# Kernel optimization log

Measured on AMD Instinct MI355X. Metric: run time of the kernel, lower is better.

## Reference

```python
import jax, jax.numpy as jnp
import numpy as np

D = 1024
NHEAD = 16
HEAD_DIM = D // NHEAD


def setup_inputs() -> dict:
    key = jax.random.key(0)
    ks = jax.random.split(key, 7)
    B, L = 4, 2048
    q = jax.random.normal(ks[0], (B, L, D), dtype=jnp.float32)
    k = jax.random.normal(ks[1], (B, L, D), dtype=jnp.float32)
    v = jax.random.normal(ks[2], (B, L, D), dtype=jnp.float32)
    # packed QKV projection, as in nn.MultiheadAttention (in_proj_weight: [3d, d])
    scale = 1.0 / np.sqrt(D)
    in_proj_w = jax.random.uniform(ks[3], (3 * D, D), dtype=jnp.float32, minval=-scale, maxval=scale)
    in_proj_b = jnp.zeros((3 * D,), dtype=jnp.float32)
    out_w = jax.random.uniform(ks[4], (D, D), dtype=jnp.float32, minval=-scale, maxval=scale)
    out_b = jnp.zeros((D,), dtype=jnp.float32)
    return {"q": q, "k": k, "v": v, "in_proj_w": in_proj_w, "in_proj_b": in_proj_b,
            "out_w": out_w, "out_b": out_b}


def reference(q, k, v, in_proj_w, in_proj_b, out_w, out_b):
    # FP32 MHA, need_weights=True (average over heads), eval mode (dropout inactive).
    B, Lq, d = q.shape
    Lk = k.shape[1]
    # packed in-projection: rows [0:d] -> Q, [d:2d] -> K, [2d:3d] -> V
    qp = q @ in_proj_w[:d].T + in_proj_b[:d]
    kp = k @ in_proj_w[d:2 * d].T + in_proj_b[d:2 * d]
    vp = v @ in_proj_w[2 * d:].T + in_proj_b[2 * d:]
    # split heads: [B, H, L, hd]
    qp = qp.reshape(B, Lq, NHEAD, HEAD_DIM).transpose(0, 2, 1, 3)
    kp = kp.reshape(B, Lk, NHEAD, HEAD_DIM).transpose(0, 2, 1, 3)
    vp = vp.reshape(B, Lk, NHEAD, HEAD_DIM).transpose(0, 2, 1, 3)
    scores = jnp.einsum('bhqd,bhkd->bhqk', qp, kp) / jnp.sqrt(jnp.float32(HEAD_DIM))
    attn = jax.nn.softmax(scores, axis=-1)          # [B, H, Lq, Lk]
    ctx = jnp.einsum('bhqk,bhkd->bhqd', attn, vp)    # [B, H, Lq, hd]
    ctx = ctx.transpose(0, 2, 1, 3).reshape(B, Lq, d)
    out = ctx @ out_w.T + out_b                      # [B, Lq, d]
    weights = attn.mean(axis=1)                      # average over heads -> [B, Lq, Lk]
    return out, weights
```

## Files before the change

### kernel.cpp

```cpp
#include <hip/hip_runtime.h>
#include <hip/hip_bf16.h>

#define D_ 1024
#define NH 16
#define HD 64
#define B_ 4
#define L_ 2048
#define N_ (B_*L_)
#define BH_ (B_*NH)
#define QSCALE_ 0.18033688011112042f

typedef __bf16 bf16_t;
typedef __bf16 bf16x4 __attribute__((ext_vector_type(4)));
typedef __bf16 bf16x8 __attribute__((ext_vector_type(8)));
typedef float f32x4 __attribute__((ext_vector_type(4)));

typedef const __attribute__((address_space(1))) char gas_t;
typedef __attribute__((address_space(3))) char las_t;

__device__ __forceinline__ f32x4 mfma_bf16(bf16x8 a, bf16x8 b, f32x4 c) {
    return __builtin_amdgcn_mfma_f32_16x16x32_bf16(a, b, c, 0, 0, 0);
}

__device__ __forceinline__ bf16x8 cvt8_f32(const float* __restrict__ p) {
    const float4* p4 = reinterpret_cast<const float4*>(p);
    float4 a = p4[0], b = p4[1];
    bf16x8 r;
    r[0] = (bf16_t)a.x; r[1] = (bf16_t)a.y; r[2] = (bf16_t)a.z; r[3] = (bf16_t)a.w;
    r[4] = (bf16_t)b.x; r[5] = (bf16_t)b.y; r[6] = (bf16_t)b.z; r[7] = (bf16_t)b.w;
    return r;
}

__device__ __forceinline__ bf16x8 ld8_bf16(const bf16_t* __restrict__ p) {
    return *reinterpret_cast<const bf16x8*>(p);
}

__global__ __launch_bounds__(256) void k_cvt_all(
    const float* __restrict__ s0, const float* __restrict__ s1,
    const float* __restrict__ s2, const float* __restrict__ sw,
    const float* __restrict__ so,
    bf16_t* __restrict__ d0, bf16_t* __restrict__ d1, bf16_t* __restrict__ d2,
    bf16_t* __restrict__ dw, bf16_t* __restrict__ dow)
{
    const int n8  = N_ * D_ / 8;
    const int n8w = 3 * D_ * D_ / 8;
    const int n8o = D_ * D_ / 8;
    const int tot = 3 * n8 + n8w + n8o;
    int i = blockIdx.x * blockDim.x + threadIdx.x;
    int stride = gridDim.x * blockDim.x;
    for (; i < tot; i += stride) {
        const float* s; bf16_t* d; int off;
        if (i < 3 * n8) {
            int seg = i >> 20; off = i & (n8 - 1);
            s = (seg == 0) ? s0 : ((seg == 1) ? s1 : s2);
            d = (seg == 0) ? d0 : ((seg == 1) ? d1 : d2);
        } else if (i < 3 * n8 + n8w) {
            off = i - 3 * n8; s = sw; d = dw;
        } else {
            off = i - 3 * n8 - n8w; s = so; d = dow;
        }
        *reinterpret_cast<bf16x8*>(d + (size_t)off * 8) = cvt8_f32(s + (size_t)off * 8);
    }
}

__global__ __launch_bounds__(256, 4) void k_gemm_qkv(
    const bf16_t* __restrict__ qb, const bf16_t* __restrict__ kb,
    const bf16_t* __restrict__ vb, const bf16_t* __restrict__ wb,
    const float* __restrict__ bias,
    bf16_t* __restrict__ qp, bf16_t* __restrict__ kp, bf16_t* __restrict__ vpT)
{
    __shared__ __align__(16) char ldsA[2][8192];
    __shared__ __align__(16) char ldsB[2][8192];
    int tid  = threadIdx.x;
    int lane = tid & 63, w = tid >> 6;
    int r = lane & 15, g = lane >> 4;
    int wr = w >> 1, wc = w & 1;

    int bid   = blockIdx.x;
    int xcd   = bid & 7;
    int seq   = bid >> 3;
    int sec   = seq >> 6;
    int inner = seq & 63;
    int tm  = xcd * 8 + (inner >> 3);
    int ctl = (inner & 7) * 128;

    const bf16_t* A = (sec == 0) ? qb : ((sec == 1) ? kb : vb);
    const bf16_t* Ab = A + (size_t)tm * 128 * 1024;
    const bf16_t* Bb = wb + (size_t)sec * D_ * D_ + (size_t)ctl * 1024;

    f32x4 z = {0.f, 0.f, 0.f, 0.f};
    f32x4 acc[4][4];
    #pragma unroll
    for (int m = 0; m < 4; ++m)
        #pragma unroll
        for (int n = 0; n < 4; ++n) acc[m][n] = z;

    auto stage = [&](int buf, int k0) {
        #pragma unroll
        for (int i = 0; i < 2; ++i) {
            int idx = i * 256 + tid;
            int row = idx >> 2;
            int lc  = (idx & 3) ^ ((row >> 1) & 3);
            const bf16_t* gA = Ab + (size_t)row * 1024 + k0 + lc * 8;
            const bf16_t* gB = Bb + (size_t)row * 1024 + k0 + lc * 8;
            __builtin_amdgcn_global_load_lds((gas_t*)gA,
                (las_t*)(&ldsA[buf][0] + idx * 16), 16, 0, 0);
            __builtin_amdgcn_global_load_lds((gas_t*)gB,
                (las_t*)(&ldsB[buf][0] + idx * 16), 16, 0, 0);
        }
    };

    stage(0, 0);
    stage(1, 32);
    int buf = 0;

    for (int k0 = 0; k0 < 1024; k0 += 32) {
        if (k0 < 992) asm volatile("s_waitcnt vmcnt(4)" ::: "memory");
        else          asm volatile("s_waitcnt vmcnt(0)" ::: "memory");
        __builtin_amdgcn_s_barrier();
        __builtin_amdgcn_sched_barrier(0);

        bf16x8 af[4], bf_[4];
        #pragma unroll
        for (int m = 0; m < 4; ++m) {
            int R = wr * 64 + m * 16 + r;
            af[m] = *reinterpret_cast<const bf16x8*>(
                &ldsA[buf][0] + R * 64 + (((g ^ ((R >> 1) & 3)) << 4)));
        }
        #pragma unroll
        for (int n = 0; n < 4; ++n) {
            int R = wc * 64 + n * 16 + r;
            bf_[n] = *reinterpret_cast<const bf16x8*>(
                &ldsB[buf][0] + R * 64 + (((g ^ ((R >> 1) & 3)) << 4)));
        }
        #pragma unroll
        for (int m = 0; m < 4; ++m)
            #pragma unroll
            for (int n = 0; n < 4; ++n)
                acc[m][n] = mfma_bf16(af[m], bf_[n], acc[m][n]);

        __builtin_amdgcn_s_barrier();
        if (k0 + 64 < 1024) stage(buf, k0 + 64);
        buf ^= 1;
    }

    #pragma unroll
    for (int m = 0; m < 4; ++m)
        #pragma unroll
        for (int n = 0; n < 4; ++n)
            #pragma unroll
            for (int i = 0; i < 4; ++i) {
                int row = tm * 128 + wr * 64 + m * 16 + g * 4 + i;
                int col = ctl + wc * 64 + n * 16 + r;
                float val = acc[m][n][i] + bias[sec * 1024 + col];
                int bb = row >> 11, ln = row & 2047;
                int h = col >> 6, dd = col & 63;
                if (sec == 0)
                    qp[(((size_t)(bb * NH + h)) * L_ + ln) * HD + dd] =
                        (bf16_t)(val * QSCALE_);
                else if (sec == 1)
                    kp[(((size_t)(bb * NH + h)) * L_ + ln) * HD + dd] = (bf16_t)val;
                else
                    vpT[(((size_t)(bb * NH + h)) * HD + dd) * L_ + ln] = (bf16_t)val;
            }
}

__global__ __launch_bounds__(256, 4) void k_gemm_out(
    const bf16_t* __restrict__ A, const bf16_t* __restrict__ Bm,
    const float* __restrict__ bias, float* __restrict__ dst)
{
    __shared__ __align__(16) char ldsA[2][8192];
    __shared__ __align__(16) char ldsB[2][8192];
    int tid  = threadIdx.x;
    int lane = tid & 63, w = tid >> 6;
    int r = lane & 15, g = lane >> 4;
    int wr = w >> 1, wc = w & 1;

    int bid = blockIdx.x;
    int swz = (bid & 7) * 64 + (bid >> 3);
    int tm = swz >> 3, tn = swz & 7;

    const bf16_t* Ab = A  + (size_t)tm * 128 * 1024;
    const bf16_t* Bb = Bm + (size_t)tn * 128 * 1024;

    f32x4 z = {0.f, 0.f, 0.f, 0.f};
    f32x4 acc[4][4];
    #pragma unroll
    for (int m = 0; m < 4; ++m)
        #pragma unroll
        for (int n = 0; n < 4; ++n) acc[m][n] = z;

    auto stage = [&](int buf, int k0) {
        #pragma unroll
        for (int i = 0; i < 2; ++i) {
            int idx = i * 256 + tid;
            int row = idx >> 2;
            int lc  = (idx & 3) ^ ((row >> 1) & 3);
            const bf16_t* gA = Ab + (size_t)row * 1024 + k0 + lc * 8;
            const bf16_t* gB = Bb + (size_t)row * 1024 + k0 + lc * 8;
            __builtin_amdgcn_global_load_lds((gas_t*)gA,
                (las_t*)(&ldsA[buf][0] + idx * 16), 16, 0, 0);
            __builtin_amdgcn_global_load_lds((gas_t*)gB,
                (las_t*)(&ldsB[buf][0] + idx * 16), 16, 0, 0);
        }
    };

    stage(0, 0);
    stage(1, 32);
    int buf = 0;

    for (int k0 = 0; k0 < 1024; k0 += 32) {
        if (k0 < 992) asm volatile("s_waitcnt vmcnt(4)" ::: "memory");
        else          asm volatile("s_waitcnt vmcnt(0)" ::: "memory");
        __builtin_amdgcn_s_barrier();
        __builtin_amdgcn_sched_barrier(0);

        bf16x8 af[4], bf_[4];
        #pragma unroll
        for (int m = 0; m < 4; ++m) {
            int R = wr * 64 + m * 16 + r;
            af[m] = *reinterpret_cast<const bf16x8*>(
                &ldsA[buf][0] + R * 64 + (((g ^ ((R >> 1) & 3)) << 4)));
        }
        #pragma unroll
        for (int n = 0; n < 4; ++n) {
            int R = wc * 64 + n * 16 + r;
            bf_[n] = *reinterpret_cast<const bf16x8*>(
                &ldsB[buf][0] + R * 64 + (((g ^ ((R >> 1) & 3)) << 4)));
        }
        #pragma unroll
        for (int m = 0; m < 4; ++m)
            #pragma unroll
            for (int n = 0; n < 4; ++n)
                acc[m][n] = mfma_bf16(af[m], bf_[n], acc[m][n]);

        __builtin_amdgcn_s_barrier();
        if (k0 + 64 < 1024) stage(buf, k0 + 64);
        buf ^= 1;
    }

    #pragma unroll
    for (int m = 0; m < 4; ++m)
        #pragma unroll
        for (int n = 0; n < 4; ++n)
            #pragma unroll
            for (int i = 0; i < 4; ++i) {
                int row = tm * 128 + wr * 64 + m * 16 + g * 4 + i;
                int col = tn * 128 + wc * 64 + n * 16 + r;
                dst[(size_t)row * 1024 + col] = acc[m][n][i] + bias[col];
            }
}

__global__ __launch_bounds__(256, 4) void k_attn(
    const bf16_t* __restrict__ qp, const bf16_t* __restrict__ kp,
    const bf16_t* __restrict__ vpT,
    bf16_t* __restrict__ ctx, float* __restrict__ lInvOut)
{
    __shared__ __align__(16) char sK[8192];
    __shared__ __align__(16) char sV[8192];
    __shared__ __align__(16) char sP[4][4096];

    int tid  = threadIdx.x;
    int w    = tid >> 6;
    int lane = tid & 63;
    int r = lane & 15, g = lane >> 4;
    int bh = blockIdx.x & 63;
    int qg = blockIdx.x >> 6;
    int qbase = qg * 128 + w * 32;

    const bf16_t* qpb = qp  + (size_t)bh * L_ * HD;
    const bf16_t* kpb = kp  + (size_t)bh * L_ * HD;
    const bf16_t* vtb = vpT + (size_t)bh * HD * L_;

    bf16x8 bq[2][2];
    #pragma unroll
    for (int qt = 0; qt < 2; ++qt)
        #pragma unroll
        for (int ds = 0; ds < 2; ++ds)
            bq[qt][ds] = ld8_bf16(qpb + (size_t)(qbase + qt * 16 + r) * HD + ds * 32 + g * 8);

    bf16x8 ones;
    #pragma unroll
    for (int i = 0; i < 8; ++i) ones[i] = (bf16_t)1.0f;

    f32x4 z = {0.f, 0.f, 0.f, 0.f};
    f32x4 acc[2][4];
    #pragma unroll
    for (int qt = 0; qt < 2; ++qt)
        #pragma unroll
        for (int dt = 0; dt < 4; ++dt) acc[qt][dt] = z;
    f32x4 acc_l[2];
    acc_l[0] = z; acc_l[1] = z;

    char* Pw = &sP[w][0];

    int srow = tid >> 3;
    int slc  = (tid & 7) ^ (srow & 7);
    const bf16_t* gK0 = kpb + (size_t)srow * HD + slc * 8;
    const bf16_t* gV0 = vtb + (size_t)srow * L_ + slc * 8;

    for (int kt = 0; kt < 32; ++kt) {
        int k0 = kt * 64;
        const bf16_t* gK = gK0 + (size_t)k0 * HD;
        const bf16_t* gV = gV0 + k0;
        #pragma unroll
        for (int i = 0; i < 2; ++i) {
            __builtin_amdgcn_global_load_lds((gas_t*)(gK + (size_t)i * 32 * HD),
                (las_t*)(&sK[0] + i * 4096 + tid * 16), 16, 0, 0);
            __builtin_amdgcn_global_load_lds((gas_t*)(gV + (size_t)i * 32 * L_),
                (las_t*)(&sV[0] + i * 4096 + tid * 16), 16, 0, 0);
        }
        __syncthreads();

        f32x4 sT[4][2];
        __builtin_amdgcn_s_setprio(1);
        #pragma unroll
        for (int ktile = 0; ktile < 4; ++ktile) {
            bf16x8 a0 = *reinterpret_cast<const bf16x8*>(
                &sK[0] + (ktile * 16 + r) * 128 + (((g    ) ^ (r & 7)) << 4));
            bf16x8 a1 = *reinterpret_cast<const bf16x8*>(
                &sK[0] + (ktile * 16 + r) * 128 + (((4 + g) ^ (r & 7)) << 4));
            #pragma unroll
            for (int qt = 0; qt < 2; ++qt) {
                f32x4 t = mfma_bf16(a0, bq[qt][0], z);
                sT[ktile][qt] = mfma_bf16(a1, bq[qt][1], t);
            }
        }
        __builtin_amdgcn_s_setprio(0);

        #pragma unroll
        for (int qt = 0; qt < 2; ++qt) {
            #pragma unroll
            for (int ktile = 0; ktile < 4; ++ktile) {
                bf16x4 pw;
                #pragma unroll
                for (int i = 0; i < 4; ++i)
                    pw[i] = (bf16_t)__builtin_amdgcn_exp2f(sT[ktile][qt][i]);
                *reinterpret_cast<bf16x4*>(Pw + (qt * 16 + r) * 128 +
                    (((2 * ktile + (g >> 1)) ^ (r & 7)) << 4) + ((g & 1) << 3)) = pw;
            }
        }

        bf16x8 pa[2][2];
        #pragma unroll
        for (int qt = 0; qt < 2; ++qt)
            #pragma unroll
            for (int ks = 0; ks < 2; ++ks)
                pa[qt][ks] = *reinterpret_cast<const bf16x8*>(
                    Pw + (qt * 16 + r) * 128 + (((4 * ks + g) ^ (r & 7)) << 4));
        __builtin_amdgcn_s_setprio(1);
        #pragma unroll
        for (int qt = 0; qt < 2; ++qt) {
            acc_l[qt] = mfma_bf16(pa[qt][0], ones, acc_l[qt]);
            acc_l[qt] = mfma_bf16(pa[qt][1], ones, acc_l[qt]);
        }
        #pragma unroll
        for (int dt = 0; dt < 4; ++dt)
            #pragma unroll
            for (int ks = 0; ks < 2; ++ks) {
                bf16x8 bv = *reinterpret_cast<const bf16x8*>(
                    &sV[0] + (dt * 16 + r) * 128 + (((4 * ks + g) ^ (r & 7)) << 4));
                acc[0][dt] = mfma_bf16(pa[0][ks], bv, acc[0][dt]);
                acc[1][dt] = mfma_bf16(pa[1][ks], bv, acc[1][dt]);
            }
        __builtin_amdgcn_s_setprio(0);

        __syncthreads();
    }

    int bb = bh >> 4, h = bh & 15;
    #pragma unroll
    for (int qt = 0; qt < 2; ++qt) {
        float lq[4];
        #pragma unroll
        for (int i = 0; i < 4; ++i) lq[i] = 1.0f / acc_l[qt][i];
        #pragma unroll
        for (int i = 0; i < 4; ++i) {
            int q = qbase + qt * 16 + 4 * g + i;
            #pragma unroll
            for (int dt = 0; dt < 4; ++dt) {
                float val = acc[qt][dt][i] * lq[i];
                ctx[(((size_t)(bb * L_ + q)) * NH + h) * HD + dt * 16 + r] = (bf16_t)val;
            }
        }
        if (r == 0) {
            #pragma unroll
            for (int i = 0; i < 4; ++i) {
                int q = qbase + qt * 16 + 4 * g + i;
                lInvOut[(size_t)bh * L_ + q] = lq[i];
            }
        }
    }
}

__global__ __launch_bounds__(256, 2) void k_weights(
    const bf16_t* __restrict__ qp, const bf16_t* __restrict__ kp,
    const float* __restrict__ lInv, float* __restrict__ wout)
{
    __shared__ __align__(16) char sQ[2][16384];
    __shared__ __align__(16) char sKt[2][16384];
    __shared__ __align__(16) float sLi[16][128];

    int tid  = threadIdx.x;
    int w    = tid >> 6;
    int lane = tid & 63;
    int r = lane & 15, g = lane >> 4;
    int wr = w >> 1, wc = w & 1;

    int wgid = (blockIdx.x & 7) * 128 + (blockIdx.x >> 3);
    int chunk = wgid >> 7;
    int b  = chunk >> 1;
    int qh = chunk & 1;
    int rem = wgid & 127;
    int qt = qh * 8 + (rem >> 4);
    int kt = rem & 15;
    int q0 = qt * 128, k0 = kt * 128;

    #pragma unroll
    for (int i = 0; i < 2; ++i) {
        int idx = i * 256 + tid;
        int h   = idx >> 5;
        int off = (idx & 31) * 4;
        const float* gl = lInv + ((size_t)(b * NH + h) * L_ + q0 + off);
        __builtin_amdgcn_global_load_lds((gas_t*)gl,
            (las_t*)((char*)&sLi[0][0] + i * 4096 + w * 1024), 16, 0, 0);
    }

    auto stage_qk = [&](int buf, int h) {
        const bf16_t* Qh = qp + ((size_t)(b * NH + h) * L_ + q0) * HD;
        const bf16_t* Kh = kp + ((size_t)(b * NH + h) * L_ + k0) * HD;
        #pragma unroll
        for (int i = 0; i < 4; ++i) {
            int idx = i * 256 + tid;
            int row = idx >> 3;
            int lc  = (idx & 7) ^ (row & 7);
            const bf16_t* gQ = Qh + (size_t)row * HD + lc * 8;
            const bf16_t* gK = Kh + (size_t)row * HD + lc * 8;
            __builtin_amdgcn_global_load_lds((gas_t*)gQ,
                (las_t*)(&sQ[buf][0]  + i * 4096 + w * 1024), 16, 0, 0);
            __builtin_amdgcn_global_load_lds((gas_t*)gK,
                (las_t*)(&sKt[buf][0] + i * 4096 + w * 1024), 16, 0, 0);
        }
    };

    float acc[4][4][4] = {};
    f32x4 z = {0.f, 0.f, 0.f, 0.f};

    stage_qk(0, 0);
    __syncthreads();
    int buf = 0;

    for (int h = 0; h < NH; ++h) {
        if (h + 1 < NH) stage_qk(buf ^ 1, h + 1);

        const char* Qb = &sQ[buf][0];
        const char* Kb = &sKt[buf][0];

        bf16x8 bfrag[4][2];
        #pragma unroll
        for (int nf = 0; nf < 4; ++nf) {
            int R = wc * 64 + nf * 16 + r;
            bfrag[nf][0] = *reinterpret_cast<const bf16x8*>(
                Kb + R * 128 + (((g    ) ^ (R & 7)) << 4));
            bfrag[nf][1] = *reinterpret_cast<const bf16x8*>(
                Kb + R * 128 + (((4 + g) ^ (R & 7)) << 4));
        }
        #pragma unroll
        for (int mf = 0; mf < 4; ++mf) {
            int R = wr * 64 + mf * 16 + r;
            bf16x8 af0 = *reinterpret_cast<const bf16x8*>(
                Qb + R * 128 + (((g    ) ^ (R & 7)) << 4));
            bf16x8 af1 = *reinterpret_cast<const bf16x8*>(
                Qb + R * 128 + (((4 + g) ^ (R & 7)) << 4));
            int qrow = wr * 64 + mf * 16 + g * 4;
            f32x4 liv = *reinterpret_cast<const f32x4*>(&sLi[h][qrow]);
            #pragma unroll
            for (int nf = 0; nf < 4; ++nf) {
                f32x4 t = mfma_bf16(af0, bfrag[nf][0], z);
                t = mfma_bf16(af1, bfrag[nf][1], t);
                #pragma unroll
                for (int i = 0; i < 4; ++i)
                    acc[mf][nf][i] += __builtin_amdgcn_exp2f(t[i]) * liv[i];
            }
        }
        __syncthreads();
        buf ^= 1;
    }

    const float inv_h = 1.0f / (float)NH;
    #pragma unroll
    for (int mf = 0; mf < 4; ++mf)
        #pragma unroll
        for (int nf = 0; nf < 4; ++nf)
            #pragma unroll
            for (int i = 0; i < 4; ++i) {
                int qidx = q0 + wr * 64 + mf * 16 + g * 4 + i;
                int kidx = k0 + wc * 64 + nf * 16 + r;
                wout[((size_t)(b * L_ + qidx)) * L_ + kidx] = acc[mf][nf][i] * inv_h;
            }
}

extern "C" void kernel_launch(void* const* d_in, const int* in_sizes, int n_in,
                              void* d_out, int out_size, void* d_ws, size_t ws_size,
                              hipStream_t stream) {
    const float* q     = (const float*)d_in[0];
    const float* k     = (const float*)d_in[1];
    const float* v     = (const float*)d_in[2];
    const float* in_w  = (const float*)d_in[3];
    const float* in_b  = (const float*)d_in[4];
    const float* out_w = (const float*)d_in[5];
    const float* out_b = (const float*)d_in[6];

    char* ws = (char*)d_ws;
    bf16_t* xb   = (bf16_t*)(ws);
    bf16_t* wb   = (bf16_t*)(ws + ((size_t)48 << 20));
    bf16_t* owb  = (bf16_t*)(ws + ((size_t)54 << 20));
    bf16_t* qp   = (bf16_t*)(ws + ((size_t)56 << 20));
    bf16_t* kp   = (bf16_t*)(ws + ((size_t)72 << 20));
    bf16_t* vpT  = (bf16_t*)(ws + ((size_t)88 << 20));
    bf16_t* ctx  = (bf16_t*)(ws + ((size_t)104 << 20));
    float*  lBuf = (float*)(ws + ((size_t)120 << 20));

    bf16_t* qb = xb;
    bf16_t* kb = xb + (size_t)N_ * D_;
    bf16_t* vb = xb + (size_t)2 * N_ * D_;

    float* outp = (float*)d_out;
    float* wout = outp + (size_t)N_ * D_;

    k_cvt_all<<<2048, 256, 0, stream>>>(q, k, v, in_w, out_w, qb, kb, vb, wb, owb);

    k_gemm_qkv<<<1536, 256, 0, stream>>>(qb, kb, vb, wb, in_b, qp, kp, vpT);

    k_attn   <<<1024, 256, 0, stream>>>(qp, kp, vpT, ctx, lBuf);
    k_weights<<<1024, 256, 0, stream>>>(qp, kp, lBuf, wout);

    k_gemm_out<<<512, 256, 0, stream>>>(ctx, owb, out_b, outp);
}
```

Measured before the change: 265.4 us.

## Merge head-averaged weights kernel and output projection GEMM into one launch

The head-averaged attention-weights kernel and the output-projection GEMM now run as one kernel of 1536 blocks. Blocks are split by index modulo 3: two of every three compute weight tiles and the third computes an output GEMM tile, all from a single shared-memory buffer. This removes one launch and the tail of each kernel, since the two independent workloads can overlap on the GPU. In exchange, every block reserves the larger 72KB LDS footprint, which may lower occupancy for the GEMM blocks, and the two register budgets are combined in one kernel.

```diff
diff --git a/kernel.cpp b/kernel.cpp
--- a/kernel.cpp
+++ b/kernel.cpp
@@ -165,92 +165,6 @@
             }
 }
 
-__global__ __launch_bounds__(256, 4) void k_gemm_out(
-    const bf16_t* __restrict__ A, const bf16_t* __restrict__ Bm,
-    const float* __restrict__ bias, float* __restrict__ dst)
-{
-    __shared__ __align__(16) char ldsA[2][8192];
-    __shared__ __align__(16) char ldsB[2][8192];
-    int tid  = threadIdx.x;
-    int lane = tid & 63, w = tid >> 6;
-    int r = lane & 15, g = lane >> 4;
-    int wr = w >> 1, wc = w & 1;
-
-    int bid = blockIdx.x;
-    int swz = (bid & 7) * 64 + (bid >> 3);
-    int tm = swz >> 3, tn = swz & 7;
-
-    const bf16_t* Ab = A  + (size_t)tm * 128 * 1024;
-    const bf16_t* Bb = Bm + (size_t)tn * 128 * 1024;
-
-    f32x4 z = {0.f, 0.f, 0.f, 0.f};
-    f32x4 acc[4][4];
-    #pragma unroll
-    for (int m = 0; m < 4; ++m)
-        #pragma unroll
-        for (int n = 0; n < 4; ++n) acc[m][n] = z;
-
-    auto stage = [&](int buf, int k0) {
-        #pragma unroll
-        for (int i = 0; i < 2; ++i) {
-            int idx = i * 256 + tid;
-            int row = idx >> 2;
-            int lc  = (idx & 3) ^ ((row >> 1) & 3);
-            const bf16_t* gA = Ab + (size_t)row * 1024 + k0 + lc * 8;
-            const bf16_t* gB = Bb + (size_t)row * 1024 + k0 + lc * 8;
-            __builtin_amdgcn_global_load_lds((gas_t*)gA,
-                (las_t*)(&ldsA[buf][0] + idx * 16), 16, 0, 0);
-            __builtin_amdgcn_global_load_lds((gas_t*)gB,
-                (las_t*)(&ldsB[buf][0] + idx * 16), 16, 0, 0);
-        }
-    };
-
-    stage(0, 0);
-    stage(1, 32);
-    int buf = 0;
-
-    for (int k0 = 0; k0 < 1024; k0 += 32) {
-        if (k0 < 992) asm volatile("s_waitcnt vmcnt(4)" ::: "memory");
-        else          asm volatile("s_waitcnt vmcnt(0)" ::: "memory");
-        __builtin_amdgcn_s_barrier();
-        __builtin_amdgcn_sched_barrier(0);
-
-        bf16x8 af[4], bf_[4];
-        #pragma unroll
-        for (int m = 0; m < 4; ++m) {
-            int R = wr * 64 + m * 16 + r;
-            af[m] = *reinterpret_cast<const bf16x8*>(
-                &ldsA[buf][0] + R * 64 + (((g ^ ((R >> 1) & 3)) << 4)));
-        }
-        #pragma unroll
-        for (int n = 0; n < 4; ++n) {
-            int R = wc * 64 + n * 16 + r;
-            bf_[n] = *reinterpret_cast<const bf16x8*>(
-                &ldsB[buf][0] + R * 64 + (((g ^ ((R >> 1) & 3)) << 4)));
-        }
-        #pragma unroll
-        for (int m = 0; m < 4; ++m)
-            #pragma unroll
-            for (int n = 0; n < 4; ++n)
-                acc[m][n] = mfma_bf16(af[m], bf_[n], acc[m][n]);
-
-        __builtin_amdgcn_s_barrier();
-        if (k0 + 64 < 1024) stage(buf, k0 + 64);
-        buf ^= 1;
-    }
-
-    #pragma unroll
-    for (int m = 0; m < 4; ++m)
-        #pragma unroll
-        for (int n = 0; n < 4; ++n)
-            #pragma unroll
-            for (int i = 0; i < 4; ++i) {
-                int row = tm * 128 + wr * 64 + m * 16 + g * 4 + i;
-                int col = tn * 128 + wc * 64 + n * 16 + r;
-                dst[(size_t)row * 1024 + col] = acc[m][n][i] + bias[col];
-            }
-}
-
 __global__ __launch_bounds__(256, 4) void k_attn(
     const bf16_t* __restrict__ qp, const bf16_t* __restrict__ kp,
     const bf16_t* __restrict__ vpT,
@@ -393,13 +307,13 @@
     }
 }
 
-__global__ __launch_bounds__(256, 2) void k_weights(
+__global__ __launch_bounds__(256, 2) void k_wo(
     const bf16_t* __restrict__ qp, const bf16_t* __restrict__ kp,
-    const float* __restrict__ lInv, float* __restrict__ wout)
+    const float* __restrict__ lInv, float* __restrict__ wout,
+    const bf16_t* __restrict__ ctxA, const bf16_t* __restrict__ owb,
+    const float* __restrict__ obias, float* __restrict__ outp)
 {
-    __shared__ __align__(16) char sQ[2][16384];
-    __shared__ __align__(16) char sKt[2][16384];
-    __shared__ __align__(16) float sLi[16][128];
+    __shared__ __align__(16) char smem[73728];
 
     int tid  = threadIdx.x;
     int w    = tid >> 6;
@@ -407,97 +321,183 @@
     int r = lane & 15, g = lane >> 4;
     int wr = w >> 1, wc = w & 1;
 
-    int wgid = (blockIdx.x & 7) * 128 + (blockIdx.x >> 3);
-    int chunk = wgid >> 7;
-    int b  = chunk >> 1;
-    int qh = chunk & 1;
-    int rem = wgid & 127;
-    int qt = qh * 8 + (rem >> 4);
-    int kt = rem & 15;
-    int q0 = qt * 128, k0 = kt * 128;
-
-    #pragma unroll
-    for (int i = 0; i < 2; ++i) {
-        int idx = i * 256 + tid;
-        int h   = idx >> 5;
-        int off = (idx & 31) * 4;
-        const float* gl = lInv + ((size_t)(b * NH + h) * L_ + q0 + off);
-        __builtin_amdgcn_global_load_lds((gas_t*)gl,
-            (las_t*)((char*)&sLi[0][0] + i * 4096 + w * 1024), 16, 0, 0);
+    int bid   = blockIdx.x;
+    int third = bid % 3;
+    int grp   = bid / 3;
+    f32x4 z = {0.f, 0.f, 0.f, 0.f};
+
+    if (third < 2) {
+        int wi = grp * 2 + third;
+        char*  sQm  = smem;
+        char*  sKm  = smem + 32768;
+        float* sLi  = (float*)(smem + 65536);
+
+        int wgid = (wi & 7) * 128 + (wi >> 3);
+        int chunk = wgid >> 7;
+        int b  = chunk >> 1;
+        int qh = chunk & 1;
+        int rem = wgid & 127;
+        int qt = qh * 8 + (rem >> 4);
+        int kt = rem & 15;
+        int q0 = qt * 128, k0 = kt * 128;
+
+        #pragma unroll
+        for (int i = 0; i < 2; ++i) {
+            int idx = i * 256 + tid;
+            int h   = idx >> 5;
+            int off = (idx & 31) * 4;
+            const float* gl = lInv + ((size_t)(b * NH + h) * L_ + q0 + off);
+            __builtin_amdgcn_global_load_lds((gas_t*)gl,
+                (las_t*)((char*)sLi + i * 4096 + w * 1024), 16, 0, 0);
+        }
+
+        auto stage_qk = [&](int buf, int h) {
+            const bf16_t* Qh = qp + ((size_t)(b * NH + h) * L_ + q0) * HD;
+            const bf16_t* Kh = kp + ((size_t)(b * NH + h) * L_ + k0) * HD;
+            #pragma unroll
+            for (int i = 0; i < 4; ++i) {
+                int idx = i * 256 + tid;
+                int row = idx >> 3;
+                int lc  = (idx & 7) ^ (row & 7);
+                const bf16_t* gQ = Qh + (size_t)row * HD + lc * 8;
+                const bf16_t* gK = Kh + (size_t)row * HD + lc * 8;
+                __builtin_amdgcn_global_load_lds((gas_t*)gQ,
+                    (las_t*)(sQm + buf * 16384 + i * 4096 + w * 1024), 16, 0, 0);
+                __builtin_amdgcn_global_load_lds((gas_t*)gK,
+                    (las_t*)(sKm + buf * 16384 + i * 4096 + w * 1024), 16, 0, 0);
+            }
+        };
+
+        float acc[4][4][4] = {};
+        stage_qk(0, 0);
+        __syncthreads();
+        int buf = 0;
+
+        for (int h = 0; h < NH; ++h) {
+            if (h + 1 < NH) stage_qk(buf ^ 1, h + 1);
+
+            const char* Qb = sQm + buf * 16384;
+            const char* Kb = sKm + buf * 16384;
+
+            bf16x8 bfrag[4][2];
+            #pragma unroll
+            for (int nf = 0; nf < 4; ++nf) {
+                int R = wc * 64 + nf * 16 + r;
+                bfrag[nf][0] = *reinterpret_cast<const bf16x8*>(
+                    Kb + R * 128 + (((g    ) ^ (R & 7)) << 4));
+                bfrag[nf][1] = *reinterpret_cast<const bf16x8*>(
+                    Kb + R * 128 + (((4 + g) ^ (R & 7)) << 4));
+            }
+            #pragma unroll
+            for (int mf = 0; mf < 4; ++mf) {
+                int R = wr * 64 + mf * 16 + r;
+                bf16x8 af0 = *reinterpret_cast<const bf16x8*>(
+                    Qb + R * 128 + (((g    ) ^ (R & 7)) << 4));
+                bf16x8 af1 = *reinterpret_cast<const bf16x8*>(
+                    Qb + R * 128 + (((4 + g) ^ (R & 7)) << 4));
+                int qrow = wr * 64 + mf * 16 + g * 4;
+                f32x4 liv = *reinterpret_cast<const f32x4*>(&sLi[qrow] + h * 128);
+                #pragma unroll
+                for (int nf = 0; nf < 4; ++nf) {
+                    f32x4 t = mfma_bf16(af0, bfrag[nf][0], z);
+                    t = mfma_bf16(af1, bfrag[nf][1], t);
+                    #pragma unroll
+                    for (int i = 0; i < 4; ++i)
+                        acc[mf][nf][i] += __builtin_amdgcn_exp2f(t[i]) * liv[i];
+                }
+            }
+            __syncthreads();
+            buf ^= 1;
+        }
+
+        const float inv_h = 1.0f / (float)NH;
+        #pragma unroll
+        for (int mf = 0; mf < 4; ++mf)
+            #pragma unroll
+            for (int nf = 0; nf < 4; ++nf)
+                #pragma unroll
+                for (int i = 0; i < 4; ++i) {
+                    int qidx = q0 + wr * 64 + mf * 16 + g * 4 + i;
+                    int kidx = k0 + wc * 64 + nf * 16 + r;
+                    wout[((size_t)(b * L_ + qidx)) * L_ + kidx] = acc[mf][nf][i] * inv_h;
+                }
+    } else {
+        int oi = grp;
+        char* ldsA0 = smem;
+        char* ldsB0 = smem + 16384;
+
+        int swz = (oi & 7) * 64 + (oi >> 3);
+        int tm = swz >> 3, tn = swz & 7;
+
+        const bf16_t* Ab = ctxA + (size_t)tm * 128 * 1024;
+        const bf16_t* Bb = owb  + (size_t)tn * 128 * 1024;
+
+        f32x4 acc[4][4];
+        #pragma unroll
+        for (int m = 0; m < 4; ++m)
+            #pragma unroll
+            for (int n = 0; n < 4; ++n) acc[m][n] = z;
+
+        auto stage = [&](int buf, int k0) {
+            #pragma unroll
+            for (int i = 0; i < 2; ++i) {
+                int idx = i * 256 + tid;
+                int row = idx >> 2;
+                int lc  = (idx & 3) ^ ((row >> 1) & 3);
+                const bf16_t* gA = Ab + (size_t)row * 1024 + k0 + lc * 8;
+                const bf16_t* gB = Bb + (size_t)row * 1024 + k0 + lc * 8;
+                __builtin_amdgcn_global_load_lds((gas_t*)gA,
+                    (las_t*)(ldsA0 + buf * 8192 + idx * 16), 16, 0, 0);
+                __builtin_amdgcn_global_load_lds((gas_t*)gB,
+                    (las_t*)(ldsB0 + buf * 8192 + idx * 16), 16, 0, 0);
+            }
+        };
+
+        stage(0, 0);
+        stage(1, 32);
+        int buf = 0;
+
+        for (int k0 = 0; k0 < 1024; k0 += 32) {
+            if (k0 < 992) asm volatile("s_waitcnt vmcnt(4)" ::: "memory");
+            else          asm volatile("s_waitcnt vmcnt(0)" ::: "memory");
+            __builtin_amdgcn_s_barrier();
+            __builtin_amdgcn_sched_barrier(0);
+
+            bf16x8 af[4], bf_[4];
+            #pragma unroll
+            for (int m = 0; m < 4; ++m) {
+                int R = wr * 64 + m * 16 + r;
+                af[m] = *reinterpret_cast<const bf16x8*>(
+                    ldsA0 + buf * 8192 + R * 64 + (((g ^ ((R >> 1) & 3)) << 4)));
+            }
+            #pragma unroll
+            for (int n = 0; n < 4; ++n) {
+                int R = wc * 64 + n * 16 + r;
+                bf_[n] = *reinterpret_cast<const bf16x8*>(
+                    ldsB0 + buf * 8192 + R * 64 + (((g ^ ((R >> 1) & 3)) << 4)));
+            }
+            #pragma unroll
+            for (int m = 0; m < 4; ++m)
+                #pragma unroll
+                for (int n = 0; n < 4; ++n)
+                    acc[m][n] = mfma_bf16(af[m], bf_[n], acc[m][n]);
+
+            __builtin_amdgcn_s_barrier();
+            if (k0 + 64 < 1024) stage(buf, k0 + 64);
+            buf ^= 1;
+        }
+
+        #pragma unroll
+        for (int m = 0; m < 4; ++m)
+            #pragma unroll
+            for (int n = 0; n < 4; ++n)
+                #pragma unroll
+                for (int i = 0; i < 4; ++i) {
+                    int row = tm * 128 + wr * 64 + m * 16 + g * 4 + i;
+                    int col = tn * 128 + wc * 64 + n * 16 + r;
+                    outp[(size_t)row * 1024 + col] = acc[m][n][i] + obias[col];
+                }
     }
-
-    auto stage_qk = [&](int buf, int h) {
-        const bf16_t* Qh = qp + ((size_t)(b * NH + h) * L_ + q0) * HD;
-        const bf16_t* Kh = kp + ((size_t)(b * NH + h) * L_ + k0) * HD;
-        #pragma unroll
-        for (int i = 0; i < 4; ++i) {
-            int idx = i * 256 + tid;
-            int row = idx >> 3;
-            int lc  = (idx & 7) ^ (row & 7);
-            const bf16_t* gQ = Qh + (size_t)row * HD + lc * 8;
-            const bf16_t* gK = Kh + (size_t)row * HD + lc * 8;
-            __builtin_amdgcn_global_load_lds((gas_t*)gQ,
-                (las_t*)(&sQ[buf][0]  + i * 4096 + w * 1024), 16, 0, 0);
-            __builtin_amdgcn_global_load_lds((gas_t*)gK,
-                (las_t*)(&sKt[buf][0] + i * 4096 + w * 1024), 16, 0, 0);
-        }
-    };
-
-    float acc[4][4][4] = {};
-    f32x4 z = {0.f, 0.f, 0.f, 0.f};
-
-    stage_qk(0, 0);
-    __syncthreads();
-    int buf = 0;
-
-    for (int h = 0; h < NH; ++h) {
-        if (h + 1 < NH) stage_qk(buf ^ 1, h + 1);
-
-        const char* Qb = &sQ[buf][0];
-        const char* Kb = &sKt[buf][0];
-
-        bf16x8 bfrag[4][2];
-        #pragma unroll
-        for (int nf = 0; nf < 4; ++nf) {
-            int R = wc * 64 + nf * 16 + r;
-            bfrag[nf][0] = *reinterpret_cast<const bf16x8*>(
-                Kb + R * 128 + (((g    ) ^ (R & 7)) << 4));
-            bfrag[nf][1] = *reinterpret_cast<const bf16x8*>(
-                Kb + R * 128 + (((4 + g) ^ (R & 7)) << 4));
-        }
-        #pragma unroll
-        for (int mf = 0; mf < 4; ++mf) {
-            int R = wr * 64 + mf * 16 + r;
-            bf16x8 af0 = *reinterpret_cast<const bf16x8*>(
-                Qb + R * 128 + (((g    ) ^ (R & 7)) << 4));
-            bf16x8 af1 = *reinterpret_cast<const bf16x8*>(
-                Qb + R * 128 + (((4 + g) ^ (R & 7)) << 4));
-            int qrow = wr * 64 + mf * 16 + g * 4;
-            f32x4 liv = *reinterpret_cast<const f32x4*>(&sLi[h][qrow]);
-            #pragma unroll
-            for (int nf = 0; nf < 4; ++nf) {
-                f32x4 t = mfma_bf16(af0, bfrag[nf][0], z);
-                t = mfma_bf16(af1, bfrag[nf][1], t);
-                #pragma unroll
-                for (int i = 0; i < 4; ++i)
-                    acc[mf][nf][i] += __builtin_amdgcn_exp2f(t[i]) * liv[i];
-            }
-        }
-        __syncthreads();
-        buf ^= 1;
-    }
-
-    const float inv_h = 1.0f / (float)NH;
-    #pragma unroll
-    for (int mf = 0; mf < 4; ++mf)
-        #pragma unroll
-        for (int nf = 0; nf < 4; ++nf)
-            #pragma unroll
-            for (int i = 0; i < 4; ++i) {
-                int qidx = q0 + wr * 64 + mf * 16 + g * 4 + i;
-                int kidx = k0 + wc * 64 + nf * 16 + r;
-                wout[((size_t)(b * L_ + qidx)) * L_ + kidx] = acc[mf][nf][i] * inv_h;
-            }
 }
 
 extern "C" void kernel_launch(void* const* d_in, const int* in_sizes, int n_in,
@@ -532,8 +532,7 @@
 
     k_gemm_qkv<<<1536, 256, 0, stream>>>(qb, kb, vb, wb, in_b, qp, kp, vpT);
 
-    k_attn   <<<1024, 256, 0, stream>>>(qp, kp, vpT, ctx, lBuf);
-    k_weights<<<1024, 256, 0, stream>>>(qp, kp, lBuf, wout);
-
-    k_gemm_out<<<512, 256, 0, stream>>>(ctx, owb, out_b, outp);
-}
+    k_attn<<<1024, 256, 0, stream>>>(qp, kp, vpT, ctx, lBuf);
+
+    k_wo<<<1536, 256, 0, stream>>>(qp, kp, lBuf, wout, ctx, owb, out_b, outp);
+}
```

Result: no change. 263.0 us (-0.9%).
